# Performance work log

Measured on AMD Instinct MI355X. Metric: run time of the kernel, lower is better.

## Reference

```python
import jax, jax.numpy as jnp
import numpy as np

B, S, D, H, DK = 2, 2048, 2048, 16, 128


def setup_inputs() -> dict:
    key = jax.random.key(0)
    k1, k2, k3 = jax.random.split(key, 3)
    hidden_states = jax.random.normal(k1, (B, S, D), dtype=jnp.float32)
    # causal multiplicative 0/1 mask [b, s, m]
    causal = jnp.tril(jnp.ones((S, S), dtype=jnp.float32))
    attention_mask = jnp.broadcast_to(causal, (B, S, S))
    qkv = jax.random.normal(k2, (D, 3, H, DK), dtype=jnp.float32) * (D ** -0.5)
    o = jax.random.normal(k3, (H, DK, D), dtype=jnp.float32) * ((H * DK) ** -0.5)
    return {"hidden_states": hidden_states, "attention_mask": attention_mask, "qkv": qkv, "o": o}


def reference(hidden_states, attention_mask, qkv, o):
    d_kernel = qkv.shape[-1]
    # _split2: project to q, k, v -> [b, h, s, dk]
    qkv_proj = jnp.einsum("bsc,cqhk->bqhsk", hidden_states, qkv)
    q, k, v = qkv_proj[:, 0], qkv_proj[:, 1], qkv_proj[:, 2]
    umask = attention_mask[:, None, :, :]  # [b, 1, s, m]
    scores = jnp.einsum("bhsk,bhmk->bhsm", q, k) * (d_kernel ** -0.5)
    scores = scores * umask - (1.0 - umask) * 10000.0
    probs = jnp.exp(jax.nn.log_softmax(scores, axis=-1))
    out = jnp.einsum("bhsm,bhmk->bshk", probs, v)
    out = jnp.einsum("bshk,hkc->bsc", out, o)
    return out
```

## Files before the change

### kernel.cpp

```cpp
#include <hip/hip_runtime.h>
#include <stdint.h>

typedef __attribute__((ext_vector_type(8))) short bf16x8;
typedef __attribute__((ext_vector_type(4))) float f32x4;
typedef __attribute__((ext_vector_type(4))) short s16x4;
typedef unsigned int u32;

#define MFMA_B16(a, b, c) __builtin_amdgcn_mfma_f32_16x16x32_bf16((a), (b), (c), 0, 0, 0)

__device__ __forceinline__ short f2b(float f) {
  u32 u = __builtin_bit_cast(u32, f);
  u32 r = (u + 0x7fffu + ((u >> 16) & 1u)) >> 16;
  return (short)(r & 0xffffu);
}

__device__ __forceinline__ void gload16(const void* g, void* l) {
  __builtin_amdgcn_global_load_lds((const __attribute__((address_space(1))) u32*)g,
                                   (__attribute__((address_space(3))) u32*)l, 16, 0, 0);
}

__global__ __launch_bounds__(256) void k_f32_to_bf16(const float* __restrict__ in,
                                                     short* __restrict__ out, int n4) {
  int i = blockIdx.x * 256 + threadIdx.x;
  if (i < n4) {
    float4 v = ((const float4*)in)[i];
    s16x4 o;
    o.x = f2b(v.x); o.y = f2b(v.y); o.z = f2b(v.z); o.w = f2b(v.w);
    ((s16x4*)out)[i] = o;
  }
}

__global__ __launch_bounds__(256) void k_transpose_bf16(const float* __restrict__ in,
                                                        short* __restrict__ out, int R, int C) {
  __shared__ short tile[32][33];
  int tx = threadIdx.x, ty = threadIdx.y;
  int x = blockIdx.x * 32 + tx;
  int y0 = blockIdx.y * 32;
#pragma unroll
  for (int k = 0; k < 4; k++)
    tile[ty + 8 * k][tx] = f2b(in[(size_t)(y0 + ty + 8 * k) * C + x]);
  __syncthreads();
  int ox = y0 + tx;
#pragma unroll
  for (int k = 0; k < 4; k++)
    out[(size_t)(blockIdx.x * 32 + ty + 8 * k) * R + ox] = tile[tx][ty + 8 * k];
}

template <int EPI>
__global__ __launch_bounds__(256, 2) void gemm_bt(const short* __restrict__ A,
                                                  const short* __restrict__ BT, int K,
                                                  void* __restrict__ out0) {
  __shared__ short As[128 * 64];
  __shared__ short Bs[128 * 64];
  const int tid = threadIdx.x;
  const int w = tid >> 6, lane = tid & 63;
  const int g = lane >> 4, c = lane & 15;
  const int wr = w >> 1, wc = w & 1;

  const int nbx = gridDim.x;
  const int id0 = blockIdx.y * nbx + blockIdx.x;
  const int per = (nbx * gridDim.y) >> 3;
  const int nid = (id0 & 7) * per + (id0 >> 3);
  const int by = nid / nbx, bx2 = nid - by * nbx;
  const int m0 = by * 128, n0 = bx2 * 128;

  f32x4 acc[4][4] = {};

  const char* APan = (const char*)(A + (size_t)m0 * K);
  const char* BPan = (const char*)(BT + (size_t)n0 * K);
  int rowA[4], cofA[4];
#pragma unroll
  for (int i = 0; i < 4; i++) {
    int ch = i * 256 + tid;
    int row = ch >> 3;
    int ci = ch & 7;
    rowA[i] = row;
    cofA[i] = (ci ^ (row & 7)) * 16;
  }
  const size_t rstride = (size_t)K * 2;
  const int nkt = K >> 6;
  for (int kt = 0; kt < nkt; ++kt) {
    const int kb = kt * 128;
#pragma unroll
    for (int i = 0; i < 4; i++) {
      gload16(APan + (size_t)rowA[i] * rstride + kb + cofA[i], (char*)As + i * 4096 + w * 1024);
      gload16(BPan + (size_t)rowA[i] * rstride + kb + cofA[i], (char*)Bs + i * 4096 + w * 1024);
    }
    __syncthreads();
    __builtin_amdgcn_s_setprio(1);
#pragma unroll
    for (int kk = 0; kk < 2; kk++) {
      bf16x8 af[4], bfr[4];
#pragma unroll
      for (int mi = 0; mi < 4; mi++) {
        int row = wr * 64 + mi * 16 + c;
        int kbyte = (kk * 64 + g * 16) ^ ((row & 7) << 4);
        af[mi] = *(const bf16x8*)((const char*)As + row * 128 + kbyte);
      }
#pragma unroll
      for (int ni = 0; ni < 4; ni++) {
        int row = wc * 64 + ni * 16 + c;
        int kbyte = (kk * 64 + g * 16) ^ ((row & 7) << 4);
        bfr[ni] = *(const bf16x8*)((const char*)Bs + row * 128 + kbyte);
      }
#pragma unroll
      for (int mi = 0; mi < 4; mi++)
#pragma unroll
        for (int ni = 0; ni < 4; ni++)
          acc[mi][ni] = MFMA_B16(af[mi], bfr[ni], acc[mi][ni]);
    }
    __builtin_amdgcn_s_setprio(0);
    __syncthreads();
  }

  if (EPI == 0) {
    short* Qb = (short*)out0;
    short* Kb = Qb + 8388608;
    short* Vt = Qb + 16777216;
#pragma unroll
    for (int ni = 0; ni < 4; ni++) {
      int n = n0 + wc * 64 + ni * 16 + c;
      int qq = n >> 11, hh = (n >> 7) & 15, dk = n & 127;
#pragma unroll
      for (int mi = 0; mi < 4; mi++) {
#pragma unroll
        for (int r = 0; r < 4; r++) {
          int m = m0 + wr * 64 + mi * 16 + g * 4 + r;
          int b = m >> 11, s = m & 2047;
          int bh = b * 16 + hh;
          short bv = f2b(acc[mi][ni][r]);
          if (qq == 0)
            Qb[((size_t)bh * 2048 + s) * 128 + dk] = bv;
          else if (qq == 1)
            Kb[((size_t)bh * 2048 + s) * 128 + dk] = bv;
          else
            Vt[((size_t)bh * 128 + dk) * 2048 + s] = bv;
        }
      }
    }
  } else {
    float* Co = (float*)out0;
#pragma unroll
    for (int ni = 0; ni < 4; ni++) {
      int n = n0 + wc * 64 + ni * 16 + c;
#pragma unroll
      for (int mi = 0; mi < 4; mi++) {
#pragma unroll
        for (int r = 0; r < 4; r++) {
          int m = m0 + wr * 64 + mi * 16 + g * 4 + r;
          Co[(size_t)m * 2048 + n] = acc[mi][ni][r];
        }
      }
    }
  }
}

__global__ __launch_bounds__(256, 2) void attn_fwd(const short* __restrict__ Qb,
                                                   const short* __restrict__ Kb,
                                                   const short* __restrict__ VTb,
                                                   short* __restrict__ Ob) {
  __shared__ short Ks[64 * 128];
  __shared__ short Vs[128 * 64];
  __shared__ short Ps[4][16][72];
  const int tid = threadIdx.x, w = tid >> 6, lane = tid & 63;
  const int g = lane >> 4, c = lane & 15;

  const int id0 = blockIdx.y * gridDim.x + blockIdx.x;
  const int nid = (id0 & 7) * 64 + (id0 >> 3);
  const int bx = nid & 15, bh = nid >> 4;

  const short* Qg = Qb + (size_t)bh * 2048 * 128;
  const short* Kg = Kb + (size_t)bh * 2048 * 128;
  const short* Vg = VTb + (size_t)bh * 128 * 2048;
  const int b = bh >> 4, hh = bh & 15;
  const float scale = 0.08838834764831845f;

  for (int pass = 0; pass < 2; ++pass) {
    const int qi = pass ? 31 - bx : bx;
    const int qs = qi * 64;

    bf16x8 qf[4];
    const int qrow = qs + w * 16 + c;
#pragma unroll
    for (int kc = 0; kc < 4; kc++)
      qf[kc] = *(const bf16x8*)(Qg + (size_t)qrow * 128 + kc * 32 + g * 8);

    float m_r[4], l_r[4];
    f32x4 accO[8];
#pragma unroll
    for (int r = 0; r < 4; r++) { m_r[r] = -INFINITY; l_r[r] = 0.f; }
#pragma unroll
    for (int nt = 0; nt < 8; nt++) accO[nt] = (f32x4){0.f, 0.f, 0.f, 0.f};

    for (int j = 0; j <= qi; ++j) {
      const int js = j * 64;
#pragma unroll
      for (int i = 0; i < 4; i++) {
        int ch = i * 256 + tid;
        {
          int row = ch >> 4, ci = ch & 15;
          int cis = ci ^ (row & 7);
          gload16(Kg + (size_t)(js + row) * 128 + cis * 8, (char*)Ks + i * 4096 + w * 1024);
        }
        {
          int row = ch >> 3, ci = ch & 7;
          int cis = ci ^ (row & 7);
          gload16(Vg + (size_t)row * 2048 + js + cis * 8, (char*)Vs + i * 4096 + w * 1024);
        }
      }
      __syncthreads();

      f32x4 accS[4] = {};
      __builtin_amdgcn_s_setprio(1);
#pragma unroll
      for (int t = 0; t < 4; t++) {
#pragma unroll
        for (int kc = 0; kc < 4; kc++) {
          int row = t * 16 + c;
          int kbyte = (kc * 64 + g * 16) ^ ((row & 7) << 4);
          bf16x8 kf = *(const bf16x8*)((const char*)Ks + row * 256 + kbyte);
          accS[t] = MFMA_B16(qf[kc], kf, accS[t]);
        }
      }
      __builtin_amdgcn_s_setprio(0);

      const bool diag = (j == qi);
      float sv[4][4];
#pragma unroll
      for (int t = 0; t < 4; t++)
#pragma unroll
        for (int r = 0; r < 4; r++) {
          float v = accS[t][r] * scale;
          if (diag) {
            int mcol = js + t * 16 + c;
            int srow = qs + w * 16 + g * 4 + r;
            if (mcol > srow) v = -1e30f;
          }
          sv[t][r] = v;
        }

#pragma unroll
      for (int r = 0; r < 4; r++) {
        float mx = fmaxf(fmaxf(sv[0][r], sv[1][r]), fmaxf(sv[2][r], sv[3][r]));
#pragma unroll
        for (int o = 8; o >= 1; o >>= 1) mx = fmaxf(mx, __shfl_xor(mx, o));
        if (mx - m_r[r] > 8.f) {
          float mnew = fmaxf(m_r[r], mx);
          float alpha = __expf(m_r[r] - mnew);
          l_r[r] *= alpha;
#pragma unroll
          for (int nt = 0; nt < 8; nt++) accO[nt][r] *= alpha;
          m_r[r] = mnew;
        }
        float rs = 0.f;
#pragma unroll
        for (int t = 0; t < 4; t++) {
          float p = __expf(sv[t][r] - m_r[r]);
          sv[t][r] = p;
          rs += p;
        }
#pragma unroll
        for (int o = 8; o >= 1; o >>= 1) rs += __shfl_xor(rs, o);
        l_r[r] += rs;
      }

#pragma unroll
      for (int t = 0; t < 4; t++)
#pragma unroll
        for (int r = 0; r < 4; r++) Ps[w][g * 4 + r][t * 16 + c] = f2b(sv[t][r]);

      __builtin_amdgcn_s_setprio(1);
#pragma unroll
      for (int kc2 = 0; kc2 < 2; kc2++) {
        bf16x8 pf = *(const bf16x8*)(&Ps[w][c][kc2 * 32 + g * 8]);
#pragma unroll
        for (int nt = 0; nt < 8; nt++) {
          int row = nt * 16 + c;
          int mbyte = (kc2 * 64 + g * 16) ^ ((row & 7) << 4);
          bf16x8 vf = *(const bf16x8*)((const char*)Vs + row * 128 + mbyte);
          accO[nt] = MFMA_B16(pf, vf, accO[nt]);
        }
      }
      __builtin_amdgcn_s_setprio(0);
      __syncthreads();
    }

#pragma unroll
    for (int r = 0; r < 4; r++) {
      float inv = 1.f / l_r[r];
      int s = qs + w * 16 + g * 4 + r;
      size_t base = ((size_t)b * 2048 + s) * 2048 + hh * 128;
#pragma unroll
      for (int nt = 0; nt < 8; nt++) {
        int kcol = nt * 16 + c;
        Ob[base + kcol] = f2b(accO[nt][r] * inv);
      }
    }
  }
}

extern "C" void kernel_launch(void* const* d_in, const int* in_sizes, int n_in, void* d_out,
                              int out_size, void* d_ws, size_t ws_size, hipStream_t stream) {
  (void)in_sizes; (void)n_in; (void)out_size; (void)ws_size;
  const float* hidden = (const float*)d_in[0];
  const float* qkvw = (const float*)d_in[2];
  const float* ow = (const float*)d_in[3];

  char* ws = (char*)d_ws;
  short* hiddenB = (short*)(ws);
  short* qkvT = (short*)(ws + 16777216);
  short* oT = (short*)(ws + 16777216);
  short* Qb = (short*)(ws + 41943040);
  short* attnO = (short*)(ws);

  k_f32_to_bf16<<<dim3(8192), dim3(256), 0, stream>>>(hidden, hiddenB, 2097152);
  k_transpose_bf16<<<dim3(192, 64), dim3(32, 8), 0, stream>>>(qkvw, qkvT, 2048, 6144);
  gemm_bt<0><<<dim3(48, 32), dim3(256), 0, stream>>>(hiddenB, qkvT, 2048, (void*)Qb);
  k_transpose_bf16<<<dim3(64, 64), dim3(32, 8), 0, stream>>>(ow, oT, 2048, 2048);
  attn_fwd<<<dim3(16, 32), dim3(256), 0, stream>>>(Qb, Qb + 8388608, Qb + 16777216, attnO);
  gemm_bt<1><<<dim3(16, 32), dim3(256), 0, stream>>>(attnO, oT, 2048, d_out);
}
```

Measured before the change: 439.4 us.

## Add 256x256-tile 512-thread QKV GEMM with 4-stage direct-to-LDS pipeline

Replaces the generic 128x128 gemm_bt used for the QKV projection with a dedicated kernel. It uses 256x256 output tiles, 8 waves and a 4-slot LDS ring filled through global_load_lds, with setprio raised around the MFMA block. The larger tile raises arithmetic intensity per LDS byte and cuts redundant global traffic, and the deeper prefetch is meant to hide load latency. In exchange it uses 128KB of LDS per block, which limits occupancy to one block per CU, and the last iterations prefetch past the K range into memory that is never used.

```diff
diff --git a/kernel.cpp b/kernel.cpp
--- a/kernel.cpp
+++ b/kernel.cpp
@@ -44,6 +44,109 @@
 #pragma unroll
   for (int k = 0; k < 4; k++)
     out[(size_t)(blockIdx.x * 32 + ty + 8 * k) * R + ox] = tile[tx][ty + 8 * k];
+}
+
+__global__ __launch_bounds__(512, 2) void gemm_qkv_256(const short* __restrict__ A,
+                                                       const short* __restrict__ BT,
+                                                       void* __restrict__ out0) {
+  __shared__ char lds[131072];
+  const int tid = threadIdx.x;
+  const int w = tid >> 6, lane = tid & 63;
+  const int g = lane >> 4, c = lane & 15;
+  const int wr = w >> 2, wc = w & 3;
+
+  const int nbx = gridDim.x;
+  const int id0 = blockIdx.y * nbx + blockIdx.x;
+  const int per = (nbx * gridDim.y) >> 3;
+  const int nid = (id0 & 7) * per + (id0 >> 3);
+  const int by = nid / nbx, bx2 = nid - by * nbx;
+  const int m0 = by * 256, n0 = bx2 * 256;
+
+  const char* APan = (const char*)(A + (size_t)m0 * 2048);
+  const char* BPan = (const char*)(BT + (size_t)n0 * 2048);
+  const size_t rstride = 4096;
+
+  int srow[2], scol[2];
+#pragma unroll
+  for (int i = 0; i < 2; i++) {
+    int chv = i * 512 + tid;
+    int r = chv >> 2;
+    srow[i] = r;
+    scol[i] = ((chv & 3) ^ (r & 3)) * 16;
+  }
+
+  f32x4 acc[8][4] = {};
+
+#define STAGE_UNIT(J)                                                                   \
+  {                                                                                     \
+    const int slot_ = (J) & 3;                                                          \
+    const int kb_ = (J) * 64;                                                           \
+    char* Ab_ = (char*)lds + slot_ * 16384;                                             \
+    char* Bb_ = (char*)lds + 65536 + slot_ * 16384;                                     \
+    gload16(APan + (size_t)srow[0] * rstride + kb_ + scol[0], Ab_ + w * 1024);          \
+    gload16(APan + (size_t)srow[1] * rstride + kb_ + scol[1], Ab_ + 8192 + w * 1024);   \
+    gload16(BPan + (size_t)srow[0] * rstride + kb_ + scol[0], Bb_ + w * 1024);          \
+    gload16(BPan + (size_t)srow[1] * rstride + kb_ + scol[1], Bb_ + 8192 + w * 1024);   \
+  }
+
+  STAGE_UNIT(0);
+  STAGE_UNIT(1);
+  STAGE_UNIT(2);
+  asm volatile("s_waitcnt vmcnt(8)" ::: "memory");
+  __builtin_amdgcn_s_barrier();
+
+  const int aoff = ((g ^ (c & 3)) * 16);
+  const int arow0 = wr * 128 + c;
+  const int brow0 = wc * 64 + c;
+
+  for (int h = 0; h < 64; ++h) {
+    const int slot = h & 3;
+    const char* Ab = (const char*)lds + slot * 16384;
+    const char* Bb = (const char*)lds + 65536 + slot * 16384;
+    bf16x8 a[8], b[4];
+#pragma unroll
+    for (int mi = 0; mi < 8; mi++)
+      a[mi] = *(const bf16x8*)(Ab + (arow0 + mi * 16) * 64 + aoff);
+#pragma unroll
+    for (int ni = 0; ni < 4; ni++)
+      b[ni] = *(const bf16x8*)(Bb + (brow0 + ni * 16) * 64 + aoff);
+    STAGE_UNIT(h + 3);
+    __builtin_amdgcn_s_setprio(1);
+#pragma unroll
+    for (int mi = 0; mi < 8; mi++)
+#pragma unroll
+      for (int ni = 0; ni < 4; ni++)
+        acc[mi][ni] = MFMA_B16(a[mi], b[ni], acc[mi][ni]);
+    __builtin_amdgcn_s_setprio(0);
+    asm volatile("s_waitcnt vmcnt(8)" ::: "memory");
+    __builtin_amdgcn_s_barrier();
+  }
+#undef STAGE_UNIT
+
+  short* Qb = (short*)out0;
+  short* Kb = Qb + 8388608;
+  short* Vt = Qb + 16777216;
+#pragma unroll
+  for (int ni = 0; ni < 4; ni++) {
+    int n = n0 + wc * 64 + ni * 16 + c;
+    int qq = n >> 11, hh = (n >> 7) & 15, dk = n & 127;
+#pragma unroll
+    for (int mi = 0; mi < 8; mi++) {
+#pragma unroll
+      for (int r = 0; r < 4; r++) {
+        int m = m0 + wr * 128 + mi * 16 + g * 4 + r;
+        int b_ = m >> 11, s = m & 2047;
+        int bh = b_ * 16 + hh;
+        short bv = f2b(acc[mi][ni][r]);
+        if (qq == 0)
+          Qb[((size_t)bh * 2048 + s) * 128 + dk] = bv;
+        else if (qq == 1)
+          Kb[((size_t)bh * 2048 + s) * 128 + dk] = bv;
+        else
+          Vt[((size_t)bh * 128 + dk) * 2048 + s] = bv;
+      }
+    }
+  }
 }
 
 template <int EPI>
@@ -315,7 +418,7 @@
 
   k_f32_to_bf16<<<dim3(8192), dim3(256), 0, stream>>>(hidden, hiddenB, 2097152);
   k_transpose_bf16<<<dim3(192, 64), dim3(32, 8), 0, stream>>>(qkvw, qkvT, 2048, 6144);
-  gemm_bt<0><<<dim3(48, 32), dim3(256), 0, stream>>>(hiddenB, qkvT, 2048, (void*)Qb);
+  gemm_qkv_256<<<dim3(24, 16), dim3(512), 0, stream>>>(hiddenB, qkvT, (void*)Qb);
   k_transpose_bf16<<<dim3(64, 64), dim3(32, 8), 0, stream>>>(ow, oT, 2048, 2048);
   attn_fwd<<<dim3(16, 32), dim3(256), 0, stream>>>(Qb, Qb + 8388608, Qb + 16777216, attnO);
   gemm_bt<1><<<dim3(16, 32), dim3(256), 0, stream>>>(attnO, oT, 2048, d_out);
```

After: 430.0 us. 1.02x faster.

## Replace GEMMs with 256x256-tile 8-wave double-buffered phased pipeline kernel

Applied to the files above, without the earlier changes.

Replaces the 128x128 single-buffer GEMM with a 512-thread kernel computing 256x256 tiles, using 128KB of LDS with double buffering and an interleaved schedule. Each k-tile is split into four MFMA phases separated by barriers, with async global-to-LDS prefetches issued between them. The goal is to overlap loads with MFMA work and to raise operand reuse. In exchange, the output projection launches only 128 blocks and the prefetch runs past the last k-tile, reading out of the tile range.

```diff
diff --git a/kernel.cpp b/kernel.cpp
--- a/kernel.cpp
+++ b/kernel.cpp
@@ -17,6 +17,12 @@
 __device__ __forceinline__ void gload16(const void* g, void* l) {
   __builtin_amdgcn_global_load_lds((const __attribute__((address_space(1))) u32*)g,
                                    (__attribute__((address_space(3))) u32*)l, 16, 0, 0);
+}
+
+__device__ __forceinline__ bf16x8 rdfrag(const char* half, int row, int ks, int g) {
+  int x = row * 128 + ks * 64 + g * 16;
+  x ^= ((x >> 9) & 1) << 5;
+  return *(const bf16x8*)(half + x);
 }
 
 __global__ __launch_bounds__(256) void k_f32_to_bf16(const float* __restrict__ in,
@@ -46,72 +52,150 @@
     out[(size_t)(blockIdx.x * 32 + ty + 8 * k) * R + ox] = tile[tx][ty + 8 * k];
 }
 
+#define STG(dstbase, Pan, hrow0, kt_)                                                    \
+  do {                                                                                   \
+    gload16((Pan) + (size_t)((hrow0) + srow0) * 4096 + (size_t)(kt_) * 128 + skb0,       \
+            (char*)lds + (dstbase) + w * 1024);                                          \
+    gload16((Pan) + (size_t)((hrow0) + 64 + srow0) * 4096 + (size_t)(kt_) * 128 + skb0,  \
+            (char*)lds + (dstbase) + 8192 + w * 1024);                                   \
+  } while (0)
+
+template <int CUR>
+__device__ __forceinline__ void tile_step(char* lds, const char* APan, const char* BPan, int T,
+                                          int w, int wr, int wc, int g, int c, int brb,
+                                          int srow0, int skb0, f32x4 (&acc)[8][4]) {
+  const char* hA = (const char*)lds + CUR * 65536 + wr * 16384;
+  const char* hB = (const char*)lds + CUR * 65536 + 32768 + (wc >> 1) * 16384;
+  const int oA = (CUR ^ 1) * 65536;
+  bf16x8 a[4][2], b0[2][2], b1[2][2];
+
+#pragma unroll
+  for (int mi = 0; mi < 4; mi++)
+#pragma unroll
+    for (int ks = 0; ks < 2; ks++) a[mi][ks] = rdfrag(hA, mi * 16 + c, ks, g);
+#pragma unroll
+  for (int ni = 0; ni < 2; ni++)
+#pragma unroll
+    for (int ks = 0; ks < 2; ks++) b0[ni][ks] = rdfrag(hB, brb + ni * 16 + c, ks, g);
+  STG(oA, APan, 0, T + 1);
+  STG(oA + 16384, APan, 128, T + 1);
+  asm volatile("s_waitcnt lgkmcnt(8)" ::: "memory");
+  __builtin_amdgcn_s_barrier();
+  asm volatile("s_waitcnt lgkmcnt(0)" ::: "memory");
+  __builtin_amdgcn_sched_barrier(0);
+  __builtin_amdgcn_s_setprio(1);
+#pragma unroll
+  for (int mi = 0; mi < 4; mi++)
+#pragma unroll
+    for (int ni = 0; ni < 2; ni++)
+#pragma unroll
+      for (int ks = 0; ks < 2; ks++) acc[mi][ni] = MFMA_B16(a[mi][ks], b0[ni][ks], acc[mi][ni]);
+  __builtin_amdgcn_s_setprio(0);
+  __builtin_amdgcn_s_barrier();
+
+#pragma unroll
+  for (int mi = 0; mi < 4; mi++)
+#pragma unroll
+    for (int ks = 0; ks < 2; ks++) a[mi][ks] = rdfrag(hA, 64 + mi * 16 + c, ks, g);
+  __builtin_amdgcn_s_barrier();
+  asm volatile("s_waitcnt lgkmcnt(0)" ::: "memory");
+  __builtin_amdgcn_sched_barrier(0);
+  __builtin_amdgcn_s_setprio(1);
+#pragma unroll
+  for (int mi = 0; mi < 4; mi++)
+#pragma unroll
+    for (int ni = 0; ni < 2; ni++)
+#pragma unroll
+      for (int ks = 0; ks < 2; ks++)
+        acc[4 + mi][ni] = MFMA_B16(a[mi][ks], b0[ni][ks], acc[4 + mi][ni]);
+  __builtin_amdgcn_s_setprio(0);
+  __builtin_amdgcn_s_barrier();
+
+#pragma unroll
+  for (int ni = 0; ni < 2; ni++)
+#pragma unroll
+    for (int ks = 0; ks < 2; ks++) b1[ni][ks] = rdfrag(hB, brb + 32 + ni * 16 + c, ks, g);
+  __builtin_amdgcn_s_barrier();
+  asm volatile("s_waitcnt lgkmcnt(0)" ::: "memory");
+  __builtin_amdgcn_sched_barrier(0);
+  __builtin_amdgcn_s_setprio(1);
+#pragma unroll
+  for (int mi = 0; mi < 4; mi++)
+#pragma unroll
+    for (int ni = 0; ni < 2; ni++)
+#pragma unroll
+      for (int ks = 0; ks < 2; ks++)
+        acc[4 + mi][2 + ni] = MFMA_B16(a[mi][ks], b1[ni][ks], acc[4 + mi][2 + ni]);
+  __builtin_amdgcn_s_setprio(0);
+  __builtin_amdgcn_s_barrier();
+
+#pragma unroll
+  for (int mi = 0; mi < 4; mi++)
+#pragma unroll
+    for (int ks = 0; ks < 2; ks++) a[mi][ks] = rdfrag(hA, mi * 16 + c, ks, g);
+  STG(CUR * 65536 + 32768, BPan, 0, T + 2);
+  STG(CUR * 65536 + 49152, BPan, 128, T + 2);
+  __builtin_amdgcn_s_barrier();
+  asm volatile("s_waitcnt lgkmcnt(0)" ::: "memory");
+  __builtin_amdgcn_sched_barrier(0);
+  __builtin_amdgcn_s_setprio(1);
+#pragma unroll
+  for (int mi = 0; mi < 4; mi++)
+#pragma unroll
+    for (int ni = 0; ni < 2; ni++)
+#pragma unroll
+      for (int ks = 0; ks < 2; ks++)
+        acc[mi][2 + ni] = MFMA_B16(a[mi][ks], b1[ni][ks], acc[mi][2 + ni]);
+  __builtin_amdgcn_s_setprio(0);
+  asm volatile("s_waitcnt vmcnt(4)" ::: "memory");
+  __builtin_amdgcn_s_barrier();
+}
+
 template <int EPI>
-__global__ __launch_bounds__(256, 2) void gemm_bt(const short* __restrict__ A,
-                                                  const short* __restrict__ BT, int K,
-                                                  void* __restrict__ out0) {
-  __shared__ short As[128 * 64];
-  __shared__ short Bs[128 * 64];
+__global__ __launch_bounds__(512, 2) void gemm_8ph(const short* __restrict__ A,
+                                                   const short* __restrict__ BT,
+                                                   void* __restrict__ out0) {
+  __shared__ char lds[131072];
   const int tid = threadIdx.x;
   const int w = tid >> 6, lane = tid & 63;
   const int g = lane >> 4, c = lane & 15;
-  const int wr = w >> 1, wc = w & 1;
+  const int wr = w >> 2, wc = w & 3;
+  const int brb = (wc & 1) * 64;
 
   const int nbx = gridDim.x;
   const int id0 = blockIdx.y * nbx + blockIdx.x;
   const int per = (nbx * gridDim.y) >> 3;
   const int nid = (id0 & 7) * per + (id0 >> 3);
   const int by = nid / nbx, bx2 = nid - by * nbx;
-  const int m0 = by * 128, n0 = bx2 * 128;
-
-  f32x4 acc[4][4] = {};
-
-  const char* APan = (const char*)(A + (size_t)m0 * K);
-  const char* BPan = (const char*)(BT + (size_t)n0 * K);
-  int rowA[4], cofA[4];
-#pragma unroll
-  for (int i = 0; i < 4; i++) {
-    int ch = i * 256 + tid;
-    int row = ch >> 3;
-    int ci = ch & 7;
-    rowA[i] = row;
-    cofA[i] = (ci ^ (row & 7)) * 16;
+  const int m0 = by * 256, n0 = bx2 * 256;
+
+  const char* APan = (const char*)(A + (size_t)m0 * 2048);
+  const char* BPan = (const char*)(BT + (size_t)n0 * 2048);
+
+  int srow0, skb0;
+  {
+    int L = tid * 16;
+    int l = L ^ (((L >> 9) & 1) << 5);
+    srow0 = l >> 7;
+    skb0 = l & 127;
   }
-  const size_t rstride = (size_t)K * 2;
-  const int nkt = K >> 6;
-  for (int kt = 0; kt < nkt; ++kt) {
-    const int kb = kt * 128;
-#pragma unroll
-    for (int i = 0; i < 4; i++) {
-      gload16(APan + (size_t)rowA[i] * rstride + kb + cofA[i], (char*)As + i * 4096 + w * 1024);
-      gload16(BPan + (size_t)rowA[i] * rstride + kb + cofA[i], (char*)Bs + i * 4096 + w * 1024);
-    }
-    __syncthreads();
-    __builtin_amdgcn_s_setprio(1);
-#pragma unroll
-    for (int kk = 0; kk < 2; kk++) {
-      bf16x8 af[4], bfr[4];
-#pragma unroll
-      for (int mi = 0; mi < 4; mi++) {
-        int row = wr * 64 + mi * 16 + c;
-        int kbyte = (kk * 64 + g * 16) ^ ((row & 7) << 4);
-        af[mi] = *(const bf16x8*)((const char*)As + row * 128 + kbyte);
-      }
-#pragma unroll
-      for (int ni = 0; ni < 4; ni++) {
-        int row = wc * 64 + ni * 16 + c;
-        int kbyte = (kk * 64 + g * 16) ^ ((row & 7) << 4);
-        bfr[ni] = *(const bf16x8*)((const char*)Bs + row * 128 + kbyte);
-      }
-#pragma unroll
-      for (int mi = 0; mi < 4; mi++)
-#pragma unroll
-        for (int ni = 0; ni < 4; ni++)
-          acc[mi][ni] = MFMA_B16(af[mi], bfr[ni], acc[mi][ni]);
-    }
-    __builtin_amdgcn_s_setprio(0);
-    __syncthreads();
+
+  f32x4 acc[8][4] = {};
+
+  STG(0, APan, 0, 0);
+  STG(16384, APan, 128, 0);
+  STG(32768, BPan, 0, 0);
+  STG(49152, BPan, 128, 0);
+  STG(65536 + 32768, BPan, 0, 1);
+  STG(65536 + 49152, BPan, 128, 1);
+  asm volatile("s_waitcnt vmcnt(4)" ::: "memory");
+  __builtin_amdgcn_s_barrier();
+
+  for (int it = 0; it < 16; ++it) {
+    tile_step<0>(lds, APan, BPan, 2 * it, w, wr, wc, g, c, brb, srow0, skb0, acc);
+    tile_step<1>(lds, APan, BPan, 2 * it + 1, w, wr, wc, g, c, brb, srow0, skb0, acc);
   }
+  asm volatile("s_waitcnt vmcnt(0)" ::: "memory");
 
   if (EPI == 0) {
     short* Qb = (short*)out0;
@@ -122,12 +206,12 @@
       int n = n0 + wc * 64 + ni * 16 + c;
       int qq = n >> 11, hh = (n >> 7) & 15, dk = n & 127;
 #pragma unroll
-      for (int mi = 0; mi < 4; mi++) {
+      for (int mi = 0; mi < 8; mi++) {
 #pragma unroll
         for (int r = 0; r < 4; r++) {
-          int m = m0 + wr * 64 + mi * 16 + g * 4 + r;
-          int b = m >> 11, s = m & 2047;
-          int bh = b * 16 + hh;
+          int m = m0 + wr * 128 + mi * 16 + g * 4 + r;
+          int b_ = m >> 11, s = m & 2047;
+          int bh = b_ * 16 + hh;
           short bv = f2b(acc[mi][ni][r]);
           if (qq == 0)
             Qb[((size_t)bh * 2048 + s) * 128 + dk] = bv;
@@ -144,10 +228,10 @@
     for (int ni = 0; ni < 4; ni++) {
       int n = n0 + wc * 64 + ni * 16 + c;
 #pragma unroll
-      for (int mi = 0; mi < 4; mi++) {
+      for (int mi = 0; mi < 8; mi++) {
 #pragma unroll
         for (int r = 0; r < 4; r++) {
-          int m = m0 + wr * 64 + mi * 16 + g * 4 + r;
+          int m = m0 + wr * 128 + mi * 16 + g * 4 + r;
           Co[(size_t)m * 2048 + n] = acc[mi][ni][r];
         }
       }
@@ -315,8 +399,8 @@
 
   k_f32_to_bf16<<<dim3(8192), dim3(256), 0, stream>>>(hidden, hiddenB, 2097152);
   k_transpose_bf16<<<dim3(192, 64), dim3(32, 8), 0, stream>>>(qkvw, qkvT, 2048, 6144);
-  gemm_bt<0><<<dim3(48, 32), dim3(256), 0, stream>>>(hiddenB, qkvT, 2048, (void*)Qb);
+  gemm_8ph<0><<<dim3(24, 16), dim3(512), 0, stream>>>(hiddenB, qkvT, (void*)Qb);
   k_transpose_bf16<<<dim3(64, 64), dim3(32, 8), 0, stream>>>(ow, oT, 2048, 2048);
   attn_fwd<<<dim3(16, 32), dim3(256), 0, stream>>>(Qb, Qb + 8388608, Qb + 16777216, attnO);
-  gemm_bt<1><<<dim3(16, 32), dim3(256), 0, stream>>>(attnO, oT, 2048, d_out);
-}
+  gemm_8ph<1><<<dim3(8, 16), dim3(512), 0, stream>>>(attnO, oT, d_out);
+}
```

Result: slower. 476.9 us (+8.5%).
